# Optimization experiments

Measured on AMD Instinct MI355X. Metric: run time of the kernel, lower is better.

Reference implementation:

```python
import jax, jax.numpy as jnp
import numpy as np

N_HEAD = 20
ALIGN_HEAD_IDX = (4, 7, 11)  # heads of alignment_heads with layer_idx == layer_index (2)


def setup_inputs() -> dict:
    key = jax.random.key(0)
    ks = jax.random.split(key, 7)
    B, Tq, Tk, D = 8, 448, 1500, 1280
    s = 1.0 / np.sqrt(D)
    return {
        "x": jax.random.normal(ks[0], (B, Tq, D), jnp.float32),
        "k": jax.random.normal(ks[1], (B, Tk, D), jnp.float32),
        "v": jax.random.normal(ks[2], (B, Tk, D), jnp.float32),
        "Wq": jax.random.normal(ks[3], (D, D), jnp.float32) * s,
        "bq": jax.random.normal(ks[4], (D,), jnp.float32) * 0.02,
        "Wo": jax.random.normal(ks[5], (D, D), jnp.float32) * s,
        "bo": jax.random.normal(ks[6], (D,), jnp.float32) * 0.02,
    }


def reference(x, k, v, Wq, bq, Wo, bo):
    B, Tq, D = x.shape
    H = N_HEAD
    Dh = D // H
    scale = Dh ** (-0.25)

    # q projection (torch Linear: x @ W.T + b)
    q = x @ Wq.T + bq                                   # [B, Tq, D]
    qh = q.reshape(B, Tq, H, Dh).transpose(0, 2, 1, 3)  # [B, H, Tq, Dh]
    kh = k.reshape(B, -1, H, Dh).transpose(0, 2, 1, 3)  # [B, H, Tk, Dh]
    vh = v.reshape(B, -1, H, Dh).transpose(0, 2, 1, 3)  # [B, H, Tk, Dh]

    # scaled QK^T, softmax in fp32
    qk = jnp.einsum("bhqd,bhkd->bhqk", qh * scale, kh * scale)
    w = jax.nn.softmax(qk.astype(jnp.float32), axis=-1).astype(q.dtype)

    out = jnp.einsum("bhqk,bhkd->bhqd", w, vh)          # [B, H, Tq, Dh]
    out = out.transpose(0, 2, 1, 3).reshape(B, Tq, D)
    out = out @ Wo.T + bo

    alignment_weights = w[:, jnp.array(ALIGN_HEAD_IDX), :, :]  # [B, 3, Tq, Tk]
    return out, alignment_weights
```

## Files before the change

kernel.cpp:

```cpp
#include <hip/hip_runtime.h>
#include <stdint.h>


typedef short bf16x8 __attribute__((ext_vector_type(8)));
typedef float f32x4  __attribute__((ext_vector_type(4)));

#define VMCNT(n) asm volatile("s_waitcnt vmcnt(" #n ")" ::: "memory")

__device__ __forceinline__ unsigned short f2bf(float f) {
  union { float f; unsigned int u; } c; c.f = f;
  unsigned int u = c.u;
  unsigned int r = (u + 0x7FFFu + ((u >> 16) & 1u)) >> 16;
  return (unsigned short)r;
}

__device__ __forceinline__ float exp2_hw(float x) {
  float r;
  asm("v_exp_f32 %0, %1" : "=v"(r) : "v"(x));
  return r;
}

__device__ __forceinline__ void gld_lds16(const void* g, void* l) {
  __builtin_amdgcn_global_load_lds(
      (__attribute__((address_space(1))) void*)g,
      (__attribute__((address_space(3))) void*)l, 16, 0, 0);
}

__device__ __forceinline__ bf16x8 ldg16(const void* p) {
  return *reinterpret_cast<const bf16x8*>(p);
}

__global__ __launch_bounds__(256) void cvt_kernel(const float* __restrict__ s0,
                                                  const float* __restrict__ s1,
                                                  const float* __restrict__ s2,
                                                  unsigned short* __restrict__ dst) {
  const int n0 = 204800, n1 = 204800;
  int i = blockIdx.x * 256 + threadIdx.x;
  const float* src; int j = i;
  if (j < n0)               { src = s0; }
  else if ((j -= n0) < n1)  { src = s1; }
  else                      { j -= n1; src = s2; }
  float4 a = *reinterpret_cast<const float4*>(src + (size_t)j * 8);
  float4 b = *reinterpret_cast<const float4*>(src + (size_t)j * 8 + 4);
  uint4 o;
  o.x = f2bf(a.x) | ((unsigned int)f2bf(a.y) << 16);
  o.y = f2bf(a.z) | ((unsigned int)f2bf(a.w) << 16);
  o.z = f2bf(b.x) | ((unsigned int)f2bf(b.y) << 16);
  o.w = f2bf(b.z) | ((unsigned int)f2bf(b.w) << 16);
  *reinterpret_cast<uint4*>(dst + (size_t)i * 8) = o;
}

__global__ __launch_bounds__(256) void kprep_kernel(const float* __restrict__ k,
                                                    unsigned short* __restrict__ kf) {
  __shared__ __attribute__((aligned(16))) char T[16 * 2568];
  const int blk = blockIdx.x;
  const int kb = blk % 96, b = blk / 96;
  const int t = threadIdx.x;

  const int r = t >> 4, cb = (t & 15) * 4;
  const int gtk = kb * 16 + r;
  const float* src = k + (size_t)(b * 1500 + (gtk < 1500 ? gtk : 0)) * 1280;
#pragma unroll
  for (int it = 0; it < 20; ++it) {
    const int c = cb + it * 64;
    float4 a = {0.f, 0.f, 0.f, 0.f};
    if (gtk < 1500) a = *reinterpret_cast<const float4*>(src + c);
    unsigned int lo = f2bf(a.x) | ((unsigned int)f2bf(a.y) << 16);
    unsigned int hi = f2bf(a.z) | ((unsigned int)f2bf(a.w) << 16);
    char* p = T + r * 2568 + c * 2;
    *reinterpret_cast<unsigned int*>(p)     = lo;
    *reinterpret_cast<unsigned int*>(p + 4) = hi;
  }
  __syncthreads();

  const int ws2 = t >> 6, l = t & 63;
#pragma unroll
  for (int i = 0; i < 10; ++i) {
    const int c = ws2 * 10 + i;
    const int h = c >> 1, h2 = c & 1;
    bf16x8 v8 = *reinterpret_cast<const bf16x8*>(
        T + (l & 15) * 2568 + h * 128 + h2 * 64 + (l >> 4) * 16);
    *reinterpret_cast<bf16x8*>(
        (char*)kf + ((((size_t)(b * 20 + h) * 96 + kb) * 2 + h2) << 10) + l * 16) = v8;
  }
}

__global__ __launch_bounds__(256) void vt_kernel(const float* __restrict__ v,
                                                 unsigned short* __restrict__ vf) {
  __shared__ __attribute__((aligned(16))) char T[128 * 132];
  int blk = blockIdx.x;
  const int kt = blk % 12; blk /= 12;
  const int h = blk % 20; const int b = blk / 20;
  const int t = threadIdx.x;
  const size_t bh = b * 20 + h;

  const int c4 = t & 15;
  const int r  = t >> 4;
#pragma unroll
  for (int p = 0; p < 8; ++p) {
    const int k = p * 16 + r;
    const int gtk = kt * 128 + k;
    float4 a = {0.f, 0.f, 0.f, 0.f};
    if (gtk < 1500)
      a = *reinterpret_cast<const float4*>(v + (size_t)(b * 1500 + gtk) * 1280 + h * 64 + c4 * 4);
    unsigned int lo = f2bf(a.x) | ((unsigned int)f2bf(a.y) << 16);
    unsigned int hi = f2bf(a.z) | ((unsigned int)f2bf(a.w) << 16);
    char* base = T + k * 132 + ((c4 ^ (k & 15)) << 3);
    *reinterpret_cast<unsigned int*>(base)     = lo;
    *reinterpret_cast<unsigned int*>(base + 4) = hi;
  }
  __syncthreads();

  const int kc8 = t & 15;
  const int kc  = kt * 4 + (kc8 >> 2);
  const int l   = (t >> 4) | ((t & 3) << 4);
#pragma unroll
  for (int p = 0; p < 4; ++p) {
    const int d = p * 16 + (t >> 4);
    unsigned short r8[8];
#pragma unroll
    for (int j = 0; j < 8; ++j) {
      const int k = kc8 * 8 + j;
      r8[j] = *reinterpret_cast<const unsigned short*>(
          T + k * 132 + (((d >> 2) ^ (k & 15)) << 3) + ((d & 3) << 1));
    }
    uint4 o;
    o.x = r8[0] | ((unsigned int)r8[1] << 16);
    o.y = r8[2] | ((unsigned int)r8[3] << 16);
    o.z = r8[4] | ((unsigned int)r8[5] << 16);
    o.w = r8[6] | ((unsigned int)r8[7] << 16);
    *reinterpret_cast<uint4*>(
        (char*)vf + (((bh * 48 + kc) * 4 + p) << 10) + l * 16) = o;
  }
}

template <int EPI>
__global__ __launch_bounds__(256) void gemm_bt(const unsigned short* __restrict__ A,
                                               const unsigned short* __restrict__ Bm,
                                               const float* __restrict__ bias,
                                               void* __restrict__ Cout,
                                               int M, int N, int K, float scale) {
  __shared__ __attribute__((aligned(16))) unsigned short As[2][128 * 64];
  __shared__ __attribute__((aligned(16))) unsigned short Bs[2][128 * 64];
  const int tid = threadIdx.x;
  const int w = tid >> 6, lane = tid & 63;
  const int l15 = lane & 15, l4 = lane >> 4;
  const int nBlk = N >> 7;
  const int cpx = gridDim.x >> 3;
  const int bid = (blockIdx.x & 7) * cpx + (blockIdx.x >> 3);
  const int bm = bid / nBlk, bn = bid % nBlk;
  const int m0 = bm << 7, n0 = bn << 7;
  const int wr = (w >> 1) << 6, wc = (w & 1) << 6;

  f32x4 acc[4][4] = {};

  auto stage = [&](int kt, int buf) {
    const int koff = kt << 6;
#pragma unroll
    for (int r = 0; r < 4; ++r) {
      const int base = (((w << 2) + r) << 10);
      const int p = base + (lane << 4);
      const int row = p >> 7;
      const int cbk = (p & 127) >> 1;
      gld_lds16(A  + ((size_t)(m0 + row) * K + koff + cbk), (char*)As[buf] + base);
      gld_lds16(Bm + ((size_t)(n0 + row) * K + koff + cbk), (char*)Bs[buf] + base);
    }
  };

  const int nKt = K >> 6;
  stage(0, 0);
  VMCNT(0);
  __builtin_amdgcn_s_barrier();

  for (int kt = 0; kt < nKt; ++kt) {
    const int buf = kt & 1;
    if (kt + 1 < nKt) {
      stage(kt + 1, buf ^ 1);
      VMCNT(8);
    } else {
      VMCNT(0);
    }
    __builtin_amdgcn_s_barrier();

    __builtin_amdgcn_s_setprio(1);
#pragma unroll
    for (int kk = 0; kk < 64; kk += 32) {
      bf16x8 af[4], bfr[4];
#pragma unroll
      for (int mi = 0; mi < 4; ++mi)
        af[mi] = *reinterpret_cast<const bf16x8*>(&As[buf][(wr + mi * 16 + l15) * 64 + kk + l4 * 8]);
#pragma unroll
      for (int ni = 0; ni < 4; ++ni)
        bfr[ni] = *reinterpret_cast<const bf16x8*>(&Bs[buf][(wc + ni * 16 + l15) * 64 + kk + l4 * 8]);
#pragma unroll
      for (int mi = 0; mi < 4; ++mi)
#pragma unroll
        for (int ni = 0; ni < 4; ++ni)
          acc[mi][ni] = __builtin_amdgcn_mfma_f32_16x16x32_bf16(af[mi], bfr[ni], acc[mi][ni], 0, 0, 0);
    }
    __builtin_amdgcn_s_setprio(0);
    __builtin_amdgcn_s_barrier();
  }

#pragma unroll
  for (int ni = 0; ni < 4; ++ni) {
    const int n = n0 + wc + ni * 16 + l15;
    const float bv = bias[n];
#pragma unroll
    for (int mi = 0; mi < 4; ++mi) {
#pragma unroll
      for (int i = 0; i < 4; ++i) {
        const int m = m0 + wr + mi * 16 + l4 * 4 + i;
        float vv = (acc[mi][ni][i] + bv) * scale;
        if (EPI == 0)
          ((unsigned short*)Cout)[(size_t)m * N + n] = f2bf(vv);
        else
          ((float*)Cout)[(size_t)m * N + n] = vv;
      }
    }
  }
}

__global__ __launch_bounds__(256, 2) void attn_kernel(const unsigned short* __restrict__ Qg,
                                                      const unsigned short* __restrict__ Kf,
                                                      const unsigned short* __restrict__ Vf,
                                                      unsigned short* __restrict__ Og,
                                                      float* __restrict__ ML) {
  __shared__ __attribute__((aligned(16))) char smem[66048];
  const int tid = threadIdx.x;
  const int w = tid >> 6, lane = tid & 63;
  const int l15 = lane & 15, l4 = lane >> 4;
  char* const Pw = smem + w * 4096;

  int bid = (blockIdx.x & 7) * 140 + (blockIdx.x >> 3);
  const int qt = bid % 7; bid /= 7;
  const int h = bid % 20; const int b = bid / 20;
  const int tq0 = qt << 6;
  const int bh = b * 20 + h;

  bf16x8 qreg[4][2];
#pragma unroll
  for (int qg = 0; qg < 4; ++qg) {
    const unsigned short* qp =
        Qg + (size_t)(b * 448 + tq0 + qg * 16 + l15) * 1280 + h * 64 + l4 * 8;
    qreg[qg][0] = ldg16(qp);
    qreg[qg][1] = ldg16(qp + 32);
  }

  const char* const Kc = (const char*)Kf + ((size_t)bh * 192 << 10) + (w << 12) + (lane << 4);
  const char* const Vc = (const char*)Vf + ((size_t)bh * 192 << 10) + (w << 12) + (lane << 4);

  bf16x8 kf[2][2], bv[4];
#pragma unroll
  for (int kg = 0; kg < 2; ++kg)
#pragma unroll
    for (int h2 = 0; h2 < 2; ++h2)
      kf[kg][h2] = ldg16(Kc + kg * 2048 + h2 * 1024);
#pragma unroll
  for (int dg = 0; dg < 4; ++dg)
    bv[dg] = ldg16(Vc + dg * 1024);

  float l_p[4] = {0.f, 0.f, 0.f, 0.f};
  f32x4 o_acc[4][4] = {};

#pragma unroll 1
  for (int kt = 0; kt < 12; ++kt) {
    bf16x8 kfn[2][2], bvn[4];
    if (kt < 11) {
      const char* kp = Kc + (kt + 1) * 16384;
      const char* vp = Vc + (kt + 1) * 16384;
#pragma unroll
      for (int kg = 0; kg < 2; ++kg)
#pragma unroll
        for (int h2 = 0; h2 < 2; ++h2)
          kfn[kg][h2] = ldg16(kp + kg * 2048 + h2 * 1024);
#pragma unroll
      for (int dg = 0; dg < 4; ++dg)
        bvn[dg] = ldg16(vp + dg * 1024);
    }

    f32x4 s[2][4] = {};
    __builtin_amdgcn_s_setprio(1);
#pragma unroll
    for (int h2 = 0; h2 < 2; ++h2) {
#pragma unroll
      for (int qg = 0; qg < 4; ++qg)
        s[0][qg] = __builtin_amdgcn_mfma_f32_16x16x32_bf16(kf[0][h2], qreg[qg][h2], s[0][qg], 0, 0, 0);
#pragma unroll
      for (int qg = 0; qg < 4; ++qg)
        s[1][qg] = __builtin_amdgcn_mfma_f32_16x16x32_bf16(kf[1][h2], qreg[qg][h2], s[1][qg], 0, 0, 0);
    }
    __builtin_amdgcn_s_setprio(0);

    if (kt == 11) {
#pragma unroll
      for (int kg = 0; kg < 2; ++kg)
#pragma unroll
        for (int i = 0; i < 4; ++i)
          if ((w << 5) + (kg << 4) + (l4 << 2) + i >= 92) {
#pragma unroll
            for (int qg = 0; qg < 4; ++qg) s[kg][qg][i] = -1e30f;
          }
    }

#pragma unroll
    for (int kg = 0; kg < 2; ++kg)
#pragma unroll
      for (int qg = 0; qg < 4; ++qg) {
#pragma unroll
        for (int i = 0; i < 4; ++i) {
          float e = exp2_hw(fmaf(s[kg][qg][i], 1.44269504f, -17.31234049f));
          s[kg][qg][i] = e;
          l_p[qg] += e;
        }
        unsigned int u0, u1;
        asm("v_cvt_pk_bf16_f32 %0, %1, %2" : "=v"(u0) : "v"(s[kg][qg][0]), "v"(s[kg][qg][1]));
        asm("v_cvt_pk_bf16_f32 %0, %1, %2" : "=v"(u1) : "v"(s[kg][qg][2]), "v"(s[kg][qg][3]));
        unsigned long long u01 = ((unsigned long long)u1 << 32) | u0;
        *reinterpret_cast<unsigned long long*>(
            Pw + (qg << 10) + (((kg << 1) + (l4 >> 1)) << 8) + (l15 << 4) + ((l4 & 1) << 3)) = u01;
      }

    __builtin_amdgcn_s_setprio(1);
#pragma unroll
    for (int qg = 0; qg < 4; ++qg) {
      bf16x8 ap = *reinterpret_cast<const bf16x8*>(Pw + (qg << 10) + (lane << 4));
#pragma unroll
      for (int dg = 0; dg < 4; ++dg)
        o_acc[qg][dg] = __builtin_amdgcn_mfma_f32_16x16x32_bf16(ap, bv[dg], o_acc[qg][dg], 0, 0, 0);
    }
    __builtin_amdgcn_s_setprio(0);

#pragma unroll
    for (int kg = 0; kg < 2; ++kg)
#pragma unroll
      for (int h2 = 0; h2 < 2; ++h2)
        kf[kg][h2] = kfn[kg][h2];
#pragma unroll
    for (int dg = 0; dg < 4; ++dg)
      bv[dg] = bvn[dg];
  }

  __syncthreads();
#pragma unroll
  for (int qg = 0; qg < 4; ++qg)
#pragma unroll
    for (int dg = 0; dg < 4; ++dg)
      *reinterpret_cast<f32x4*>(smem + (w << 14) + (((qg << 2) + dg) << 10) + (lane << 4)) =
          o_acc[qg][dg];

  float* const Lb = reinterpret_cast<float*>(smem + 65536);
  float lw[4];
#pragma unroll
  for (int qg = 0; qg < 4; ++qg) {
    float t = l_p[qg] + __shfl_xor(l_p[qg], 16);
    t += __shfl_xor(t, 32);
    lw[qg] = t;
  }
  if (l4 == 0) {
#pragma unroll
    for (int qg = 0; qg < 4; ++qg) Lb[(w << 6) + (qg << 4) + l15] = lw[qg];
  }
  __syncthreads();

  float ltot = 0.f;
#pragma unroll
  for (int w2 = 0; w2 < 4; ++w2) ltot += Lb[(w2 << 6) + (w << 4) + l15];
  const float rr = 1.f / ltot;
  float rinv4[4], lt4[4];
#pragma unroll
  for (int i = 0; i < 4; ++i) {
    rinv4[i] = __shfl(rr,   (l4 << 2) + i);
    lt4[i]   = __shfl(ltot, (l4 << 2) + i);
  }
#pragma unroll
  for (int dg = 0; dg < 4; ++dg) {
    f32x4 t = *reinterpret_cast<const f32x4*>(smem + (((w << 2) + dg) << 10) + (lane << 4));
#pragma unroll
    for (int w2 = 1; w2 < 4; ++w2)
      t += *reinterpret_cast<const f32x4*>(
          smem + (w2 << 14) + (((w << 2) + dg) << 10) + (lane << 4));
#pragma unroll
    for (int i = 0; i < 4; ++i)
      Og[(size_t)(b * 448 + tq0 + (w << 4) + (l4 << 2) + i) * 1280 + h * 64 + (dg << 4) + l15] =
          f2bf(t[i] * rinv4[i]);
  }
  if (l15 == 0) {
#pragma unroll
    for (int i = 0; i < 4; ++i) {
      size_t idx = (size_t)bh * 448 + tq0 + (w << 4) + (l4 << 2) + i;
      ML[idx * 2]     = 12.0f;
      ML[idx * 2 + 1] = lt4[i];
    }
  }
}

__global__ __launch_bounds__(256) void weights_kernel(const unsigned short* __restrict__ Qg,
                                                      const unsigned short* __restrict__ Kf,
                                                      const float* __restrict__ ML,
                                                      float* __restrict__ Wout) {
  const int tid = threadIdx.x;
  const int w = tid >> 6, lane = tid & 63;
  const int l15 = lane & 15, l4 = lane >> 4;
  int bid = (blockIdx.x & 7) * 21 + (blockIdx.x >> 3);
  const int qt = bid % 7; bid /= 7;
  const int ha = bid % 3; const int b = bid / 3;
  const int h = (ha == 0) ? 4 : (ha == 1) ? 7 : 11;
  const int tq0 = qt << 6;

  const unsigned short* qptr =
      Qg + (size_t)(b * 448 + tq0 + w * 16 + l15) * 1280 + h * 64 + l4 * 8;
  bf16x8 qreg[2];
  qreg[0] = ldg16(qptr);
  qreg[1] = ldg16(qptr + 32);

  float m_r[4], rinv[4];
#pragma unroll
  for (int i = 0; i < 4; ++i) {
    size_t idx = (size_t)(b * 20 + h) * 448 + tq0 + w * 16 + l4 * 4 + i;
    m_r[i]  = ML[idx * 2];
    rinv[i] = 1.f / ML[idx * 2 + 1];
  }
  float* wbase = Wout + ((size_t)(b * 3 + ha) * 448 + tq0) * 1500;

  const char* const Kc = (const char*)Kf +
      ((size_t)(b * 20 + h) * 192 << 10) + (lane << 4);

  bf16x8 bk[4][2];
#pragma unroll
  for (int ni = 0; ni < 4; ++ni)
#pragma unroll
    for (int h2 = 0; h2 < 2; ++h2)
      bk[ni][h2] = ldg16(Kc + ((ni * 2 + h2) << 10));

#pragma unroll 1
  for (int kt = 0; kt < 24; ++kt) {
    bf16x8 bkn[4][2];
    if (kt < 23) {
      const char* kp = Kc + (size_t)(kt + 1) * 8192;
#pragma unroll
      for (int ni = 0; ni < 4; ++ni)
#pragma unroll
        for (int h2 = 0; h2 < 2; ++h2)
          bkn[ni][h2] = ldg16(kp + ((ni * 2 + h2) << 10));
    }

    f32x4 s[4] = {};
    __builtin_amdgcn_s_setprio(1);
#pragma unroll
    for (int h2 = 0; h2 < 2; ++h2)
#pragma unroll
      for (int ni = 0; ni < 4; ++ni)
        s[ni] = __builtin_amdgcn_mfma_f32_16x16x32_bf16(qreg[h2], bk[ni][h2], s[ni], 0, 0, 0);
    __builtin_amdgcn_s_setprio(0);

    const int k0 = kt << 6;
#pragma unroll
    for (int ni = 0; ni < 4; ++ni) {
      const int col = k0 + ni * 16 + l15;
      if (col < 1500) {
#pragma unroll
        for (int i = 0; i < 4; ++i) {
          const int row = w * 16 + l4 * 4 + i;
          wbase[(size_t)row * 1500 + col] = __expf(s[ni][i] - m_r[i]) * rinv[i];
        }
      }
    }

#pragma unroll
    for (int ni = 0; ni < 4; ++ni)
#pragma unroll
      for (int h2 = 0; h2 < 2; ++h2)
        bk[ni][h2] = bkn[ni][h2];
  }
}

extern "C" void kernel_launch(void* const* d_in, const int* in_sizes, int n_in,
                              void* d_out, int out_size, void* d_ws, size_t ws_size,
                              hipStream_t stream) {
  const float* x  = (const float*)d_in[0];
  const float* k  = (const float*)d_in[1];
  const float* v  = (const float*)d_in[2];
  const float* Wq = (const float*)d_in[3];
  const float* bq = (const float*)d_in[4];
  const float* Wo = (const float*)d_in[5];
  const float* bo = (const float*)d_in[6];
  float* out  = (float*)d_out;
  float* wout = out + (size_t)8 * 448 * 1280;

  char* ws = (char*)d_ws;
  unsigned short* wqb   = (unsigned short*)(ws);
  unsigned short* wob   = (unsigned short*)(ws + 3276800);
  unsigned short* xb    = (unsigned short*)(ws + 6553600);
  unsigned short* qs    = (unsigned short*)(ws + 15728640);
  unsigned short* kfrag = (unsigned short*)(ws + 24903680);
  unsigned short* vfrag = (unsigned short*)(ws + 56360960);
  float* ml             = (float*)(ws + 87818240);
  unsigned short* ao    = xb;

  cvt_kernel<<<3840, 256, 0, stream>>>(Wq, Wo, x, wqb);
  kprep_kernel<<<768, 256, 0, stream>>>(k, kfrag);
  vt_kernel<<<1920, 256, 0, stream>>>(v, vfrag);

  gemm_bt<0><<<280, 256, 0, stream>>>(xb, wqb, bq, (void*)qs, 3584, 1280, 1280, 0.125f);

  attn_kernel<<<8 * 20 * 7, 256, 0, stream>>>(qs, kfrag, vfrag, ao, ml);

  gemm_bt<1><<<280, 256, 0, stream>>>(ao, wob, bo, (void*)out, 3584, 1280, 1280, 1.0f);

  weights_kernel<<<8 * 3 * 7, 256, 0, stream>>>(qs, kfrag, ml, wout);
}
```

Before: 194.2 us.

## Fuse prep kernels and shrink attention LDS for higher occupancy

Merges the three conversion kernels (weights/x cast, K fragment prep, V transpose) into one launch with block-range dispatch, and rewrites K prep to read directly from global without an LDS staging tile. The attention epilogue now reduces the cross-wave partial outputs one q-group at a time, which shrinks shared memory from about 66KB to 17KB and raises the launch bound from 2 to 4 blocks per CU. This is meant to cut launch overhead and improve attention occupancy, at the cost of extra barriers in the epilogue and possible register pressure under the tighter launch bound.

```diff
diff --git a/kernel.cpp b/kernel.cpp
--- a/kernel.cpp
+++ b/kernel.cpp
@@ -30,107 +30,105 @@
   return *reinterpret_cast<const bf16x8*>(p);
 }
 
-__global__ __launch_bounds__(256) void cvt_kernel(const float* __restrict__ s0,
-                                                  const float* __restrict__ s1,
-                                                  const float* __restrict__ s2,
-                                                  unsigned short* __restrict__ dst) {
-  const int n0 = 204800, n1 = 204800;
-  int i = blockIdx.x * 256 + threadIdx.x;
-  const float* src; int j = i;
-  if (j < n0)               { src = s0; }
-  else if ((j -= n0) < n1)  { src = s1; }
-  else                      { j -= n1; src = s2; }
-  float4 a = *reinterpret_cast<const float4*>(src + (size_t)j * 8);
-  float4 b = *reinterpret_cast<const float4*>(src + (size_t)j * 8 + 4);
-  uint4 o;
-  o.x = f2bf(a.x) | ((unsigned int)f2bf(a.y) << 16);
-  o.y = f2bf(a.z) | ((unsigned int)f2bf(a.w) << 16);
-  o.z = f2bf(b.x) | ((unsigned int)f2bf(b.y) << 16);
-  o.w = f2bf(b.z) | ((unsigned int)f2bf(b.w) << 16);
-  *reinterpret_cast<uint4*>(dst + (size_t)i * 8) = o;
-}
-
-__global__ __launch_bounds__(256) void kprep_kernel(const float* __restrict__ k,
-                                                    unsigned short* __restrict__ kf) {
-  __shared__ __attribute__((aligned(16))) char T[16 * 2568];
-  const int blk = blockIdx.x;
-  const int kb = blk % 96, b = blk / 96;
-  const int t = threadIdx.x;
-
-  const int r = t >> 4, cb = (t & 15) * 4;
-  const int gtk = kb * 16 + r;
-  const float* src = k + (size_t)(b * 1500 + (gtk < 1500 ? gtk : 0)) * 1280;
-#pragma unroll
-  for (int it = 0; it < 20; ++it) {
-    const int c = cb + it * 64;
-    float4 a = {0.f, 0.f, 0.f, 0.f};
-    if (gtk < 1500) a = *reinterpret_cast<const float4*>(src + c);
-    unsigned int lo = f2bf(a.x) | ((unsigned int)f2bf(a.y) << 16);
-    unsigned int hi = f2bf(a.z) | ((unsigned int)f2bf(a.w) << 16);
-    char* p = T + r * 2568 + c * 2;
-    *reinterpret_cast<unsigned int*>(p)     = lo;
-    *reinterpret_cast<unsigned int*>(p + 4) = hi;
-  }
-  __syncthreads();
-
-  const int ws2 = t >> 6, l = t & 63;
-#pragma unroll
-  for (int i = 0; i < 10; ++i) {
-    const int c = ws2 * 10 + i;
-    const int h = c >> 1, h2 = c & 1;
-    bf16x8 v8 = *reinterpret_cast<const bf16x8*>(
-        T + (l & 15) * 2568 + h * 128 + h2 * 64 + (l >> 4) * 16);
-    *reinterpret_cast<bf16x8*>(
-        (char*)kf + ((((size_t)(b * 20 + h) * 96 + kb) * 2 + h2) << 10) + l * 16) = v8;
-  }
-}
-
-__global__ __launch_bounds__(256) void vt_kernel(const float* __restrict__ v,
-                                                 unsigned short* __restrict__ vf) {
+__global__ __launch_bounds__(256) void prep_kernel(
+    const float* __restrict__ x,  const float* __restrict__ Wq,
+    const float* __restrict__ Wo, const float* __restrict__ k,
+    const float* __restrict__ v,
+    unsigned short* __restrict__ cvtdst,
+    unsigned short* __restrict__ kf,
+    unsigned short* __restrict__ vf) {
   __shared__ __attribute__((aligned(16))) char T[128 * 132];
   int blk = blockIdx.x;
-  const int kt = blk % 12; blk /= 12;
-  const int h = blk % 20; const int b = blk / 20;
   const int t = threadIdx.x;
-  const size_t bh = b * 20 + h;
-
-  const int c4 = t & 15;
-  const int r  = t >> 4;
-#pragma unroll
-  for (int p = 0; p < 8; ++p) {
-    const int k = p * 16 + r;
-    const int gtk = kt * 128 + k;
-    float4 a = {0.f, 0.f, 0.f, 0.f};
-    if (gtk < 1500)
-      a = *reinterpret_cast<const float4*>(v + (size_t)(b * 1500 + gtk) * 1280 + h * 64 + c4 * 4);
-    unsigned int lo = f2bf(a.x) | ((unsigned int)f2bf(a.y) << 16);
-    unsigned int hi = f2bf(a.z) | ((unsigned int)f2bf(a.w) << 16);
-    char* base = T + k * 132 + ((c4 ^ (k & 15)) << 3);
-    *reinterpret_cast<unsigned int*>(base)     = lo;
-    *reinterpret_cast<unsigned int*>(base + 4) = hi;
-  }
-  __syncthreads();
-
-  const int kc8 = t & 15;
-  const int kc  = kt * 4 + (kc8 >> 2);
-  const int l   = (t >> 4) | ((t & 3) << 4);
-#pragma unroll
-  for (int p = 0; p < 4; ++p) {
-    const int d = p * 16 + (t >> 4);
-    unsigned short r8[8];
-#pragma unroll
-    for (int j = 0; j < 8; ++j) {
-      const int k = kc8 * 8 + j;
-      r8[j] = *reinterpret_cast<const unsigned short*>(
-          T + k * 132 + (((d >> 2) ^ (k & 15)) << 3) + ((d & 3) << 1));
-    }
+
+  if (blk < 1920) {
+    const int kt = blk % 12; blk /= 12;
+    const int h = blk % 20; const int b = blk / 20;
+    const size_t bh = b * 20 + h;
+
+    const int c4 = t & 15;
+    const int r  = t >> 4;
+#pragma unroll
+    for (int p = 0; p < 8; ++p) {
+      const int kk = p * 16 + r;
+      const int gtk = kt * 128 + kk;
+      float4 a = {0.f, 0.f, 0.f, 0.f};
+      if (gtk < 1500)
+        a = *reinterpret_cast<const float4*>(v + (size_t)(b * 1500 + gtk) * 1280 + h * 64 + c4 * 4);
+      unsigned int lo = f2bf(a.x) | ((unsigned int)f2bf(a.y) << 16);
+      unsigned int hi = f2bf(a.z) | ((unsigned int)f2bf(a.w) << 16);
+      char* base = T + kk * 132 + ((c4 ^ (kk & 15)) << 3);
+      *reinterpret_cast<unsigned int*>(base)     = lo;
+      *reinterpret_cast<unsigned int*>(base + 4) = hi;
+    }
+    __syncthreads();
+
+    const int kc8 = t & 15;
+    const int kc  = kt * 4 + (kc8 >> 2);
+    const int l   = (t >> 4) | ((t & 3) << 4);
+#pragma unroll
+    for (int p = 0; p < 4; ++p) {
+      const int d = p * 16 + (t >> 4);
+      unsigned short r8[8];
+#pragma unroll
+      for (int j = 0; j < 8; ++j) {
+        const int kk = kc8 * 8 + j;
+        r8[j] = *reinterpret_cast<const unsigned short*>(
+            T + kk * 132 + (((d >> 2) ^ (kk & 15)) << 3) + ((d & 3) << 1));
+      }
+      uint4 o;
+      o.x = r8[0] | ((unsigned int)r8[1] << 16);
+      o.y = r8[2] | ((unsigned int)r8[3] << 16);
+      o.z = r8[4] | ((unsigned int)r8[5] << 16);
+      o.w = r8[6] | ((unsigned int)r8[7] << 16);
+      *reinterpret_cast<uint4*>(
+          (char*)vf + (((bh * 48 + kc) * 4 + p) << 10) + l * 16) = o;
+    }
+    return;
+  }
+
+  if (blk < 3840) {
+    const int w = t >> 6, l = t & 63;
+    const int cbase = (blk - 1920) * 16 + w * 4;
+#pragma unroll
+    for (int i = 0; i < 4; ++i) {
+      const int c = cbase + i;
+      const int h2 = c & 1;
+      const int kb = (c >> 1) % 96;
+      const int rest = (c >> 1) / 96;
+      const int h = rest % 20, b = rest / 20;
+      const int row = kb * 16 + (l & 15);
+      float4 a = {0.f, 0.f, 0.f, 0.f}, bq4 = {0.f, 0.f, 0.f, 0.f};
+      if (row < 1500) {
+        const float* src = k + (size_t)(b * 1500 + row) * 1280 + h * 64 + h2 * 32 + (l >> 4) * 8;
+        a   = *reinterpret_cast<const float4*>(src);
+        bq4 = *reinterpret_cast<const float4*>(src + 4);
+      }
+      uint4 o;
+      o.x = f2bf(a.x)   | ((unsigned int)f2bf(a.y)   << 16);
+      o.y = f2bf(a.z)   | ((unsigned int)f2bf(a.w)   << 16);
+      o.z = f2bf(bq4.x) | ((unsigned int)f2bf(bq4.y) << 16);
+      o.w = f2bf(bq4.z) | ((unsigned int)f2bf(bq4.w) << 16);
+      *reinterpret_cast<uint4*>((char*)kf + ((size_t)c << 10) + l * 16) = o;
+    }
+    return;
+  }
+
+  {
+    const int n0 = 204800, n1 = 204800;
+    int i = (blk - 3840) * 256 + t;
+    const float* src; int j = i;
+    if (j < n0)               { src = Wq; }
+    else if ((j -= n0) < n1)  { src = Wo; }
+    else                      { j -= n1; src = x; }
+    float4 a = *reinterpret_cast<const float4*>(src + (size_t)j * 8);
+    float4 b = *reinterpret_cast<const float4*>(src + (size_t)j * 8 + 4);
     uint4 o;
-    o.x = r8[0] | ((unsigned int)r8[1] << 16);
-    o.y = r8[2] | ((unsigned int)r8[3] << 16);
-    o.z = r8[4] | ((unsigned int)r8[5] << 16);
-    o.w = r8[6] | ((unsigned int)r8[7] << 16);
-    *reinterpret_cast<uint4*>(
-        (char*)vf + (((bh * 48 + kc) * 4 + p) << 10) + l * 16) = o;
+    o.x = f2bf(a.x) | ((unsigned int)f2bf(a.y) << 16);
+    o.y = f2bf(a.z) | ((unsigned int)f2bf(a.w) << 16);
+    o.z = f2bf(b.x) | ((unsigned int)f2bf(b.y) << 16);
+    o.w = f2bf(b.z) | ((unsigned int)f2bf(b.w) << 16);
+    *reinterpret_cast<uint4*>(cvtdst + (size_t)i * 8) = o;
   }
 }
 
@@ -221,16 +219,17 @@
   }
 }
 
-__global__ __launch_bounds__(256, 2) void attn_kernel(const unsigned short* __restrict__ Qg,
+__global__ __launch_bounds__(256, 4) void attn_kernel(const unsigned short* __restrict__ Qg,
                                                       const unsigned short* __restrict__ Kf,
                                                       const unsigned short* __restrict__ Vf,
                                                       unsigned short* __restrict__ Og,
                                                       float* __restrict__ ML) {
-  __shared__ __attribute__((aligned(16))) char smem[66048];
+  __shared__ __attribute__((aligned(16))) char smem[17408];
   const int tid = threadIdx.x;
   const int w = tid >> 6, lane = tid & 63;
   const int l15 = lane & 15, l4 = lane >> 4;
   char* const Pw = smem + w * 4096;
+  float* const Lb = reinterpret_cast<float*>(smem + 16384);
 
   int bid = (blockIdx.x & 7) * 140 + (blockIdx.x >> 3);
   const int qt = bid % 7; bid /= 7;
@@ -341,57 +340,39 @@
       bv[dg] = bvn[dg];
   }
 
-  __syncthreads();
-#pragma unroll
-  for (int qg = 0; qg < 4; ++qg)
+#pragma unroll
+  for (int qg = 0; qg < 4; ++qg) {
+    float tsum = l_p[qg] + __shfl_xor(l_p[qg], 16);
+    tsum += __shfl_xor(tsum, 32);
+    if (l4 == 0) Lb[(w << 6) + (qg << 4) + l15] = tsum;
+  }
+
+#pragma unroll
+  for (int qg = 0; qg < 4; ++qg) {
 #pragma unroll
     for (int dg = 0; dg < 4; ++dg)
-      *reinterpret_cast<f32x4*>(smem + (w << 14) + (((qg << 2) + dg) << 10) + (lane << 4)) =
-          o_acc[qg][dg];
-
-  float* const Lb = reinterpret_cast<float*>(smem + 65536);
-  float lw[4];
-#pragma unroll
-  for (int qg = 0; qg < 4; ++qg) {
-    float t = l_p[qg] + __shfl_xor(l_p[qg], 16);
-    t += __shfl_xor(t, 32);
-    lw[qg] = t;
-  }
-  if (l4 == 0) {
-#pragma unroll
-    for (int qg = 0; qg < 4; ++qg) Lb[(w << 6) + (qg << 4) + l15] = lw[qg];
-  }
-  __syncthreads();
-
-  float ltot = 0.f;
-#pragma unroll
-  for (int w2 = 0; w2 < 4; ++w2) ltot += Lb[(w2 << 6) + (w << 4) + l15];
-  const float rr = 1.f / ltot;
-  float rinv4[4], lt4[4];
-#pragma unroll
-  for (int i = 0; i < 4; ++i) {
-    rinv4[i] = __shfl(rr,   (l4 << 2) + i);
-    lt4[i]   = __shfl(ltot, (l4 << 2) + i);
-  }
-#pragma unroll
-  for (int dg = 0; dg < 4; ++dg) {
-    f32x4 t = *reinterpret_cast<const f32x4*>(smem + (((w << 2) + dg) << 10) + (lane << 4));
+      *reinterpret_cast<f32x4*>(Pw + (dg << 10) + (lane << 4)) = o_acc[qg][dg];
+    __syncthreads();
+
+    f32x4 tsum = *reinterpret_cast<const f32x4*>(smem + (w << 10) + (lane << 4));
 #pragma unroll
     for (int w2 = 1; w2 < 4; ++w2)
-      t += *reinterpret_cast<const f32x4*>(
-          smem + (w2 << 14) + (((w << 2) + dg) << 10) + (lane << 4));
-#pragma unroll
-    for (int i = 0; i < 4; ++i)
-      Og[(size_t)(b * 448 + tq0 + (w << 4) + (l4 << 2) + i) * 1280 + h * 64 + (dg << 4) + l15] =
-          f2bf(t[i] * rinv4[i]);
-  }
-  if (l15 == 0) {
+      tsum += *reinterpret_cast<const f32x4*>(smem + (w2 << 12) + (w << 10) + (lane << 4));
 #pragma unroll
     for (int i = 0; i < 4; ++i) {
-      size_t idx = (size_t)bh * 448 + tq0 + (w << 4) + (l4 << 2) + i;
-      ML[idx * 2]     = 12.0f;
-      ML[idx * 2 + 1] = lt4[i];
-    }
+      const int q = (qg << 4) + (l4 << 2) + i;
+      const float ltot = Lb[q] + Lb[64 + q] + Lb[128 + q] + Lb[192 + q];
+      Og[(size_t)(b * 448 + tq0 + q) * 1280 + h * 64 + (w << 4) + l15] =
+          f2bf(tsum[i] / ltot);
+    }
+    __syncthreads();
+  }
+
+  if (w == 0) {
+    const float ltot = Lb[lane] + Lb[64 + lane] + Lb[128 + lane] + Lb[192 + lane];
+    const size_t idx = (size_t)bh * 448 + tq0 + lane;
+    ML[idx * 2]     = 12.0f;
+    ML[idx * 2 + 1] = ltot;
   }
 }
 
@@ -498,9 +479,7 @@
   float* ml             = (float*)(ws + 87818240);
   unsigned short* ao    = xb;
 
-  cvt_kernel<<<3840, 256, 0, stream>>>(Wq, Wo, x, wqb);
-  kprep_kernel<<<768, 256, 0, stream>>>(k, kfrag);
-  vt_kernel<<<1920, 256, 0, stream>>>(v, vfrag);
+  prep_kernel<<<7680, 256, 0, stream>>>(x, Wq, Wo, k, v, wqb, kfrag, vfrag);
 
   gemm_bt<0><<<280, 256, 0, stream>>>(xb, wqb, bq, (void*)qs, 3584, 1280, 1280, 0.125f);
 
```

New measurement: 471.5 us. 2.43x slower.
